# Kernel optimization log

Measured on AMD Instinct MI355X. Metric: run time of the kernel, lower is better.

## Reference

```python
import jax, jax.numpy as jnp
import numpy as np
from jax import lax


def conv2d(x, w, b=None, pad=0):
    y = lax.conv_general_dilated(x, w, (1, 1), [(pad, pad), (pad, pad)],
                                 dimension_numbers=('NCHW', 'OIHW', 'NCHW'))
    if b is not None:
        y = y + b[None, :, None, None]
    return y


def setup_inputs():
    key = jax.random.key(0)
    ks = jax.random.split(key, 8)
    B, C, H, W = 8, 3, 224, 224
    OC, NH, HD = 32, 8, 4
    s = lambda fan: 1.0 / np.sqrt(fan)
    x = jax.random.normal(ks[0], (B, C, H, W), jnp.float32)
    # gumbel noise for the hard gumbel-softmax over attention logits [B,NH,HD,H,H]
    gumbel = jax.random.gumbel(ks[1], (B, NH, HD, H, H), jnp.float32)
    in_w = jax.random.normal(ks[2], (OC, C, 3, 3), jnp.float32) * s(C * 9)
    in_b = jnp.zeros((OC,), jnp.float32)
    qkv_w = jax.random.normal(ks[3], (3 * OC, OC, 3, 3), jnp.float32) * s(OC * 9)
    proj_w = jax.random.normal(ks[4], (OC, OC, 1, 1), jnp.float32) * s(OC)
    proj_b = jnp.zeros((OC,), jnp.float32)
    upd_w = jax.random.normal(ks[5], (OC, OC, 1, 1), jnp.float32) * s(OC)
    upd_b = jnp.zeros((OC,), jnp.float32)
    bn_gamma = jnp.ones((OC,), jnp.float32)
    bn_beta = jnp.zeros((OC,), jnp.float32)
    return {"x": x, "gumbel": gumbel, "in_w": in_w, "in_b": in_b, "qkv_w": qkv_w,
            "proj_w": proj_w, "proj_b": proj_b, "upd_w": upd_w, "upd_b": upd_b,
            "bn_gamma": bn_gamma, "bn_beta": bn_beta}


def reference(x, gumbel, in_w, in_b, qkv_w, proj_w, proj_b, upd_w, upd_b, bn_gamma, bn_beta):
    B, _, H, W = x.shape
    NH, HD = 8, 4
    OC = NH * HD
    EPS = 1e-5
    x1 = conv2d(x, in_w, in_b, pad=1)                       # [B,32,H,W]
    qkv = conv2d(x1, qkv_w, None, pad=1).reshape(B, NH, 3, HD, H, W)
    q, k, v = qkv[:, :, 0], qkv[:, :, 1], qkv[:, :, 2]      # each [B,NH,HD,H,W]
    scale = HD ** -0.5
    # matmul(q, k^T) over the last two dims -> [B,NH,HD,H,H]
    logits = jnp.einsum('bndiw,bndjw->bndij', q, k) * scale
    # hard gumbel-softmax, tau=1, straight-through
    y_soft = jax.nn.softmax(logits + gumbel, axis=-1)
    idx = jnp.argmax(y_soft, axis=-1)
    y_hard = jax.nn.one_hot(idx, H, dtype=y_soft.dtype)
    att = y_hard - lax.stop_gradient(y_soft) + y_soft
    A = jnp.einsum('bndij,bndjw->bndiw', att, v).reshape(B, OC, H, W)
    # F.interpolate to (224,224) bilinear is identity since H=W=224
    A = conv2d(A, proj_w, proj_b)
    A = conv2d(A, upd_w, upd_b)
    # BatchNorm2d in training mode (batch statistics, biased variance)
    mean = A.mean(axis=(0, 2, 3), keepdims=True)
    var = ((A - mean) ** 2).mean(axis=(0, 2, 3), keepdims=True)
    A = (A - mean) * lax.rsqrt(var + EPS)
    A = A * bn_gamma[None, :, None, None] + bn_beta[None, :, None, None]
    A = A * jax.nn.sigmoid(A)  # SiLU; dropout is identity (eval)
    out = A + x1
    return out, att
```

## Files before the change

### kernel.cpp

```cpp
#include <hip/hip_runtime.h>
#include <hip/hip_bf16.h>

#define NB 8
#define CIN 3
#define HH 224
#define WW 224
#define OC 32
#define NH 8
#define HD 4
#define NHD 32
#define C96 96
#define HWSZ (HH*WW)

#define PH 226
#define PW 228
#define CHS (PH*PW)

#define HT 4
#define OCT 8
#define NGB 4

__device__ __forceinline__ void gld_lds16(const float* gsrc, float* ldst) {
    __builtin_amdgcn_global_load_lds(
        (const __attribute__((address_space(1))) uint32_t*)gsrc,
        (__attribute__((address_space(3))) uint32_t*)ldst,
        16, 0, 0);
}

__global__ void k_w2(const float* __restrict__ pw, const float* __restrict__ pb,
                     const float* __restrict__ uw, const float* __restrict__ ub,
                     float* __restrict__ W2, float* __restrict__ b2) {
    int c = threadIdx.x, o = threadIdx.y;
    float acc = 0.f;
    for (int m = 0; m < OC; ++m) acc = fmaf(uw[o*OC + m], pw[m*OC + c], acc);
    W2[o*OC + c] = acc;
    if (c == 0) {
        float bb = ub[o];
        for (int m = 0; m < OC; ++m) bb = fmaf(uw[o*OC + m], pb[m], bb);
        b2[o] = bb;
    }
}

__global__ __launch_bounds__(256) void k_conv_in_tile(const float* __restrict__ x,
                                                      const float* __restrict__ w,
                                                      const float* __restrict__ bias,
                                                      float* __restrict__ x1) {
    int h0 = blockIdx.x * 2;
    int b  = blockIdx.y;
    __shared__ float xs[CIN][4][226];
    int t = threadIdx.x;
    for (int ch = 0; ch < CIN; ++ch)
        for (int r = 0; r < 4; ++r) {
            int gh = h0 - 1 + r;
            for (int col = t; col < 226; col += 256) {
                float v = 0.f;
                if (gh >= 0 && gh < HH && col > 0 && col < 225)
                    v = x[((size_t)(b*CIN + ch)*HH + gh)*WW + (col-1)];
                xs[ch][r][col] = v;
            }
        }
    __syncthreads();
    int wv = t;
    if (wv >= WW) return;
    float xv[CIN][4][3];
    #pragma unroll
    for (int c = 0; c < CIN; ++c)
        #pragma unroll
        for (int r = 0; r < 4; ++r)
            #pragma unroll
            for (int j = 0; j < 3; ++j)
                xv[c][r][j] = xs[c][r][wv + j];
    float acc[2][OC];
    #pragma unroll
    for (int hy = 0; hy < 2; ++hy)
        for (int oc = 0; oc < OC; ++oc) acc[hy][oc] = 0.f;
    #pragma unroll
    for (int c = 0; c < CIN; ++c)
        #pragma unroll
        for (int kh = 0; kh < 3; ++kh)
            #pragma unroll
            for (int kw = 0; kw < 3; ++kw)
                for (int oc = 0; oc < OC; ++oc) {
                    float wgt = w[oc*CIN*9 + c*9 + kh*3 + kw];
                    #pragma unroll
                    for (int hy = 0; hy < 2; ++hy)
                        acc[hy][oc] = fmaf(xv[c][hy+kh][kw], wgt, acc[hy][oc]);
                }
    for (int oc = 0; oc < OC; ++oc) {
        float bs = bias[oc];
        #pragma unroll
        for (int hy = 0; hy < 2; ++hy)
            x1[((size_t)(b*OC + oc)*PH + (h0+hy+1))*PW + (wv+1)] = __fadd_rn(acc[hy][oc], bs);
    }
}

__global__ __launch_bounds__(256) void k_conv_qkv_tile(const float* __restrict__ x1g,
                                                       const float* __restrict__ w,
                                                       float* __restrict__ qk4,
                                                       float* __restrict__ vbg) {
    int h0 = blockIdx.x * HT;
    int og = blockIdx.y * OCT;
    int z  = blockIdx.z;
    const float* x1b = x1g + (size_t)z*OC*CHS;
    float* qk = qk4 + (size_t)z*64*HWSZ;
    float* vb = vbg + (size_t)z*OC*HWSZ;
    __shared__ float xs[2][1536];
    int t = threadIdx.x;
    int lane = t & 63, wid = t >> 6;
    int wv = t;
    float acc[HT][OCT];
    #pragma unroll
    for (int a = 0; a < HT; ++a)
        #pragma unroll
        for (int o = 0; o < OCT; ++o) acc[a][o] = 0.f;

    {
        const float* src = x1b + (size_t)h0*PW;
        for (int k = wid; k < 6; k += 4)
            gld_lds16(src + k*256 + lane*4, &xs[0][k*256]);
    }
    __syncthreads();

    for (int c = 0; c < OC; ++c) {
        int cur = c & 1;
        if (c + 1 < OC) {
            const float* src = x1b + (size_t)(c+1)*CHS + (size_t)h0*PW;
            float* dst = xs[cur ^ 1];
            for (int k = wid; k < 6; k += 4)
                gld_lds16(src + k*256 + lane*4, dst + k*256);
        }
        if (wv < WW) {
            float xv[HT+2][3];
            #pragma unroll
            for (int r = 0; r < HT+2; ++r)
                #pragma unroll
                for (int j = 0; j < 3; ++j)
                    xv[r][j] = xs[cur][r*PW + wv + j];
            #pragma unroll
            for (int o = 0; o < OCT; ++o) {
                const float* wr = w + ((size_t)(og + o)*OC + c)*9;
                #pragma unroll
                for (int kh = 0; kh < 3; ++kh)
                    #pragma unroll
                    for (int kw = 0; kw < 3; ++kw) {
                        float wgt = wr[kh*3 + kw];
                        #pragma unroll
                        for (int hy = 0; hy < HT; ++hy)
                            acc[hy][o] = fmaf(xv[hy+kh][kw], wgt, acc[hy][o]);
                    }
            }
        }
        __syncthreads();
    }
    if (wv < WW) {
        #pragma unroll
        for (int o = 0; o < OCT; ++o) {
            int oc = og + o;
            int n = oc / 12, rem = oc % 12;
            int r = rem >> 2, d = rem & 3;
            #pragma unroll
            for (int hy = 0; hy < HT; ++hy) {
                int h = h0 + hy;
                if (r < 2)
                    qk[((size_t)(n*8 + r*4 + d)*HH + h)*WW + wv] = acc[hy][o];
                else
                    vb[((size_t)(n*4 + d)*HH + h)*WW + wv] = acc[hy][o];
            }
        }
    }
}

__global__ __launch_bounds__(256) void k_attn_ri(const float* __restrict__ qk4,
                                                 const float* __restrict__ gum,
                                                 float* __restrict__ att,
                                                 int* __restrict__ idxout,
                                                 int b0) {
    int i0 = blockIdx.x * 8;
    int nd = blockIdx.y;
    int z  = blockIdx.z;
    int b  = b0 + z;
    const float* qkz = qk4 + (size_t)z*64*HWSZ;
    const float* gumb = gum + (size_t)b*NHD*HH*HH;
    float* attb = att + (size_t)b*NHD*HH*HH;
    int* idxb = idxout + (size_t)b*NHD*HH;
    int n = nd >> 2, d = nd & 3;
    const float* qb = qkz + ((size_t)(n*8 + d)*HH + i0)*WW;
    const float* kb = qkz + ((size_t)(n*8 + 4 + d)*HH)*WW;
    __shared__ __align__(16) float qs[8][WW];
    __shared__ float vals[8][256];
    __shared__ int   win_s[8];
    int t = threadIdx.x;
    for (int f = t; f < 8*(WW/4); f += 256) {
        int r = f / (WW/4), p = (f % (WW/4))*4;
        *(float4*)(&qs[r][p]) = *(const float4*)(qb + (size_t)r*WW + p);
    }
    __syncthreads();
    if (t < WW) {
        const float* kr = kb + (size_t)t*WW;
        float s0[8], s1[8], s2[8], s3[8];
        #pragma unroll
        for (int ii = 0; ii < 8; ++ii) { s0[ii]=0.f; s1[ii]=0.f; s2[ii]=0.f; s3[ii]=0.f; }
        for (int w = 0; w < WW; w += 4) {
            float4 kc = *(const float4*)(kr + w);
            #pragma unroll
            for (int ii = 0; ii < 8; ++ii) {
                float4 qc = *(const float4*)(&qs[ii][w]);
                s0[ii] = __fadd_rn(s0[ii], __fmul_rn(qc.x, kc.x));
                s1[ii] = __fadd_rn(s1[ii], __fmul_rn(qc.y, kc.y));
                s2[ii] = __fadd_rn(s2[ii], __fmul_rn(qc.z, kc.z));
                s3[ii] = __fadd_rn(s3[ii], __fmul_rn(qc.w, kc.w));
            }
        }
        #pragma unroll
        for (int ii = 0; ii < 8; ++ii) {
            float dot = __fadd_rn(__fadd_rn(s0[ii], s1[ii]), __fadd_rn(s2[ii], s3[ii]));
            vals[ii][t] = __fadd_rn(__fmul_rn(0.5f, dot),
                                    gumb[((size_t)nd*HH + (i0 + ii))*HH + t]);
        }
    } else {
        #pragma unroll
        for (int ii = 0; ii < 8; ++ii) vals[ii][t] = -INFINITY;
    }
    __syncthreads();
    int ii = t >> 5, jj = t & 31;
    float best = -INFINITY; int bj = 0x7fffffff;
    for (int j = jj; j < 256; j += 32) {
        float v = vals[ii][j];
        if (v > best) { best = v; bj = j; }
    }
    for (int off = 16; off > 0; off >>= 1) {
        float v2 = __shfl_down(best, off, 32);
        int   j2 = __shfl_down(bj,   off, 32);
        if (v2 > best || (v2 == best && j2 < bj)) { best = v2; bj = j2; }
    }
    if (jj == 0) { win_s[ii] = bj; idxb[nd*HH + i0 + ii] = bj; }
    __syncthreads();
    for (int e = t; e < 8*WW; e += 256) {
        int r = e / WW, j = e - r*WW;
        attb[((size_t)nd*HH + (i0 + r))*HH + j] = (j == win_s[r]) ? 1.f : 0.f;
    }
}

__global__ __launch_bounds__(256) void k_gather_mm(const float* __restrict__ vbuf,
                                                   const int* __restrict__ idx,
                                                   const float* __restrict__ W2g,
                                                   const float* __restrict__ b2g,
                                                   float* __restrict__ A2) {
    int i = blockIdx.x, b = blockIdx.y;
    __shared__ float w2s[OC*OC];
    __shared__ float b2s[OC];
    __shared__ int   id[OC];
    for (int t = threadIdx.x; t < OC*OC; t += blockDim.x) w2s[t] = W2g[t];
    if (threadIdx.x < OC) {
        b2s[threadIdx.x] = b2g[threadIdx.x];
        id[threadIdx.x]  = idx[(b*NHD + threadIdx.x)*HH + i];
    }
    __syncthreads();
    int wv = threadIdx.x;
    if (wv >= WW) return;
    float vals[OC];
    for (int c = 0; c < OC; ++c)
        vals[c] = vbuf[((size_t)(b*OC + c)*HH + id[c])*WW + wv];
    for (int oc = 0; oc < OC; ++oc) {
        float a = b2s[oc];
        for (int c = 0; c < OC; ++c) a = fmaf(w2s[oc*OC + c], vals[c], a);
        A2[((size_t)(b*OC + oc)*HH + i)*WW + wv] = a;
    }
}

__global__ __launch_bounds__(256) void k_stats(const float* __restrict__ A2,
                                               float* __restrict__ sums,
                                               float* __restrict__ sumsq) {
    int oc = blockIdx.x, s = blockIdx.y;
    int t = threadIdx.x;
    float a = 0.f, a2 = 0.f;
    const int SL = HWSZ/16;
    for (int b = 0; b < NB; ++b) {
        const float* base = A2 + (size_t)(b*OC + oc)*HWSZ + s*SL;
        for (int e = t*4; e < SL; e += 256*4) {
            float4 v = *(const float4*)(base + e);
            a  += v.x + v.y + v.z + v.w;
            a2 += v.x*v.x + v.y*v.y + v.z*v.z + v.w*v.w;
        }
    }
    __shared__ float r1[256], r2[256];
    r1[t] = a; r2[t] = a2;
    __syncthreads();
    for (int st = 128; st > 0; st >>= 1) {
        if (t < st) { r1[t] += r1[t+st]; r2[t] += r2[t+st]; }
        __syncthreads();
    }
    if (t == 0) { atomicAdd(&sums[oc], r1[0]); atomicAdd(&sumsq[oc], r2[0]); }
}

__global__ __launch_bounds__(256) void k_final(const float* __restrict__ A2,
                                               const float* __restrict__ x1,
                                               const float* __restrict__ sums,
                                               const float* __restrict__ sumsq,
                                               const float* __restrict__ gamma,
                                               const float* __restrict__ beta,
                                               float* __restrict__ out) {
    int i = blockIdx.x, b = blockIdx.y;
    __shared__ float mean_s[OC], inv_s[OC], g_s[OC], be_s[OC];
    if (threadIdx.x < OC) {
        int oc = threadIdx.x;
        const float N = (float)(NB*HH*WW);
        float mean = sums[oc]/N;
        float var  = sumsq[oc]/N - mean*mean;
        mean_s[oc] = mean;
        inv_s[oc]  = rsqrtf(var + 1e-5f);
        g_s[oc]    = gamma[oc];
        be_s[oc]   = beta[oc];
    }
    __syncthreads();
    int wv = threadIdx.x;
    if (wv >= WW) return;
    for (int oc = 0; oc < OC; ++oc) {
        size_t o = ((size_t)(b*OC + oc)*HH + i)*WW + wv;
        float a = A2[o];
        float an = (a - mean_s[oc])*inv_s[oc]*g_s[oc] + be_s[oc];
        float sw = an / (1.f + __expf(-an));
        out[o] = sw + x1[((size_t)(b*OC + oc)*PH + (i+1))*PW + (wv+1)];
    }
}

extern "C" void kernel_launch(void* const* d_in, const int* in_sizes, int n_in,
                              void* d_out, int out_size, void* d_ws, size_t ws_size,
                              hipStream_t stream) {
    const float* x      = (const float*)d_in[0];
    const float* gumbel = (const float*)d_in[1];
    const float* in_w   = (const float*)d_in[2];
    const float* in_b   = (const float*)d_in[3];
    const float* qkv_w  = (const float*)d_in[4];
    const float* proj_w = (const float*)d_in[5];
    const float* proj_b = (const float*)d_in[6];
    const float* upd_w  = (const float*)d_in[7];
    const float* upd_b  = (const float*)d_in[8];
    const float* bng    = (const float*)d_in[9];
    const float* bnb    = (const float*)d_in[10];

    float* out = (float*)d_out;
    float* att = out + (size_t)NB*OC*HWSZ;

    float* x1   = (float*)d_ws;
    float* qk4  = x1 + (size_t)NB*OC*CHS;
    float* A2   = qk4;
    float* vbuf = qk4 + (size_t)NGB*64*HWSZ;
    float* W2   = vbuf + (size_t)NB*OC*HWSZ;
    float* b2   = W2 + OC*OC;
    float* sums = b2 + OC;
    float* sumsq= sums + OC;
    int*   idx  = (int*)(sumsq + OC);

    hipMemsetAsync(x1, 0, (size_t)NB*OC*CHS*sizeof(float), stream);
    hipMemsetAsync(sums, 0, 2*OC*sizeof(float), stream);

    k_w2          <<<1, dim3(OC, OC), 0, stream>>>(proj_w, proj_b, upd_w, upd_b, W2, b2);
    k_conv_in_tile<<<dim3(HH/2, NB), 256, 0, stream>>>(x, in_w, in_b, x1);

    for (int g = 0; g < NB/NGB; ++g) {
        k_conv_qkv_tile<<<dim3(HH/HT, C96/OCT, NGB), 256, 0, stream>>>(
            x1 + (size_t)g*NGB*OC*CHS, qkv_w, qk4, vbuf + (size_t)g*NGB*OC*HWSZ);
        k_attn_ri<<<dim3(HH/8, NHD, NGB), 256, 0, stream>>>(
            qk4, gumbel, att, idx, g*NGB);
    }

    k_gather_mm<<<dim3(HH, NB), 256, 0, stream>>>(vbuf, idx, W2, b2, A2);
    k_stats    <<<dim3(OC, 16), 256, 0, stream>>>(A2, sums, sumsq);
    k_final    <<<dim3(HH, NB), 256, 0, stream>>>(A2, x1, sums, sumsq, bng, bnb, out);
}
```

Measured before the change: 827.0 us.

## Store K in a w-blocked transposed layout for coalesced attention loads

The qkv conv now writes K through an LDS transpose into a layout where each group of four w values for consecutive rows sits contiguously. Attention threads then read K with stride-4 float4 loads across rows instead of each thread walking its own row, which gives coalesced global loads. The cost is extra LDS space (larger xs buffer), an added barrier and an LDS round-trip in the conv epilogue.

```diff
diff --git a/kernel.cpp b/kernel.cpp
--- a/kernel.cpp
+++ b/kernel.cpp
@@ -19,6 +19,7 @@
 #define HT 4
 #define OCT 8
 #define NGB 4
+
 
 __device__ __forceinline__ void gld_lds16(const float* gsrc, float* ldst) {
     __builtin_amdgcn_global_load_lds(
@@ -104,7 +105,7 @@
     const float* x1b = x1g + (size_t)z*OC*CHS;
     float* qk = qk4 + (size_t)z*64*HWSZ;
     float* vb = vbg + (size_t)z*OC*HWSZ;
-    __shared__ float xs[2][1536];
+    __shared__ float xs[2][2240];
     int t = threadIdx.x;
     int lane = t & 63, wid = t >> 6;
     int wv = t;
@@ -156,15 +157,41 @@
         #pragma unroll
         for (int o = 0; o < OCT; ++o) {
             int oc = og + o;
-            int n = oc / 12, rem = oc % 12;
+            int rem = oc % 12;
             int r = rem >> 2, d = rem & 3;
-            #pragma unroll
-            for (int hy = 0; hy < HT; ++hy) {
-                int h = h0 + hy;
-                if (r < 2)
-                    qk[((size_t)(n*8 + r*4 + d)*HH + h)*WW + wv] = acc[hy][o];
-                else
-                    vb[((size_t)(n*4 + d)*HH + h)*WW + wv] = acc[hy][o];
+            int n = oc / 12;
+            if (r == 0) {
+                #pragma unroll
+                for (int hy = 0; hy < HT; ++hy)
+                    qk[((size_t)(n*8 + d)*HH + (h0+hy))*WW + wv] = acc[hy][o];
+            } else if (r == 2) {
+                #pragma unroll
+                for (int hy = 0; hy < HT; ++hy)
+                    vb[((size_t)(n*4 + d)*HH + (h0+hy))*WW + wv] = acc[hy][o];
+            }
+        }
+    }
+    int ogm = og % 12;
+    if (ogm != 8) {
+        int ko = (ogm == 0) ? 4 : 0;
+        int n  = og / 12;
+        float* kt = &xs[0][0];
+        if (wv < WW) {
+            int wb = wv >> 2, wl = wv & 3;
+            #pragma unroll
+            for (int kk = 0; kk < 4; ++kk)
+                #pragma unroll
+                for (int hy = 0; hy < HT; ++hy)
+                    kt[(kk*56 + wb)*20 + hy*4 + wl] = acc[hy][ko + kk];
+        }
+        __syncthreads();
+        if (wv < WW) {
+            int wb = wv >> 2, s = wv & 3;
+            #pragma unroll
+            for (int kk = 0; kk < 4; ++kk) {
+                float4 kvv = *(const float4*)(&kt[(kk*56 + wb)*20 + s*4]);
+                *(float4*)(qk + (size_t)(n*8 + 4 + kk)*HWSZ
+                               + (size_t)wb*(HH*4) + (size_t)(h0 + s)*4) = kvv;
             }
         }
     }
@@ -185,7 +212,7 @@
     int* idxb = idxout + (size_t)b*NHD*HH;
     int n = nd >> 2, d = nd & 3;
     const float* qb = qkz + ((size_t)(n*8 + d)*HH + i0)*WW;
-    const float* kb = qkz + ((size_t)(n*8 + 4 + d)*HH)*WW;
+    const float* kT = qkz + (size_t)(n*8 + 4 + d)*HWSZ;
     __shared__ __align__(16) float qs[8][WW];
     __shared__ float vals[8][256];
     __shared__ int   win_s[8];
@@ -196,12 +223,12 @@
     }
     __syncthreads();
     if (t < WW) {
-        const float* kr = kb + (size_t)t*WW;
         float s0[8], s1[8], s2[8], s3[8];
         #pragma unroll
         for (int ii = 0; ii < 8; ++ii) { s0[ii]=0.f; s1[ii]=0.f; s2[ii]=0.f; s3[ii]=0.f; }
+        const float* kTt = kT + (size_t)t*4;
         for (int w = 0; w < WW; w += 4) {
-            float4 kc = *(const float4*)(kr + w);
+            float4 kc = *(const float4*)(kTt + (size_t)(w >> 2)*(HH*4));
             #pragma unroll
             for (int ii = 0; ii < 8; ++ii) {
                 float4 qc = *(const float4*)(&qs[ii][w]);
```

Result: faster. 746.7 us (-9.7%).
